# Kernel tuning notes

Measured on AMD Instinct MI355X. Metric: run time of the kernel, lower is better.

## Reference

```python
import jax, jax.numpy as jnp
import numpy as np

N_EMBD = 1024
N_HEAD = 16
HEAD_SIZE = 64

def setup_inputs() -> dict:
    key = jax.random.key(0)
    ks = jax.random.split(key, 6)
    B, T = 4, 2048
    x = jax.random.normal(ks[0], (B, T, N_EMBD), dtype=jnp.float32)
    s = 1.0 / np.sqrt(N_EMBD)
    Wq = jax.random.normal(ks[1], (N_HEAD, N_EMBD, HEAD_SIZE), dtype=jnp.float32) * s
    Wk = jax.random.normal(ks[2], (N_HEAD, N_EMBD, HEAD_SIZE), dtype=jnp.float32) * s
    Wv = jax.random.normal(ks[3], (N_HEAD, N_EMBD, HEAD_SIZE), dtype=jnp.float32) * s
    Wp = jax.random.normal(ks[4], (N_EMBD, N_EMBD), dtype=jnp.float32) * s
    bp = jax.random.normal(ks[5], (N_EMBD,), dtype=jnp.float32) * 0.01
    return {"x": x, "Wq": Wq, "Wk": Wk, "Wv": Wv, "Wp": Wp, "bp": bp}

def reference(x, Wq, Wk, Wv, Wp, bp):
    B, T, C = x.shape
    # per-head projections, all heads at once: [B,H,T,hs]
    q = jnp.einsum('btc,hcd->bhtd', x, Wq)
    k = jnp.einsum('btc,hcd->bhtd', x, Wk)
    v = jnp.einsum('btc,hcd->bhtd', x, Wv)
    # NOTE: original scales by C**-0.5 with C = n_embd (not head_size)
    scale = C ** (-0.5)
    wei = jnp.einsum('bhtd,bhsd->bhts', q, k) * scale  # [B,H,T,T]
    causal = jnp.tril(jnp.ones((T, T), dtype=bool))
    wei = jnp.where(causal, wei, -jnp.inf)
    wei = jax.nn.softmax(wei, axis=-1)
    out = jnp.einsum('bhts,bhsd->bhtd', wei, v)  # [B,H,T,hs]
    out = out.transpose(0, 2, 1, 3).reshape(B, T, -1)  # concat heads -> [B,T,C]
    return out @ Wp + bp
```

## Files before the change

kernel.cpp:

```cpp
#include <hip/hip_runtime.h>
#include <stdint.h>
#include <math.h>

typedef short s16x8 __attribute__((ext_vector_type(8)));
typedef float f32x4 __attribute__((ext_vector_type(4)));
typedef float f32x16 __attribute__((ext_vector_type(16)));

__device__ __forceinline__ unsigned short f2bf(float f) {
    union { float f; uint32_t u; } x; x.f = f;
    uint32_t r = x.u + 0x7FFFu + ((x.u >> 16) & 1u);
    return (unsigned short)(r >> 16);
}

__device__ __forceinline__ uint32_t cvtpk_bf16(float lo, float hi) {
    uint32_t r;
    asm("v_cvt_pk_bf16_f32 %0, %1, %2" : "=v"(r) : "v"(lo), "v"(hi));
    return r;
}

#define GLD_LDS16(gp, lp) __builtin_amdgcn_global_load_lds( \
    (const __attribute__((address_space(1))) uint32_t*)(gp), \
    (__attribute__((address_space(3))) uint32_t*)(lp), 16, 0, 0)

#define MFMA16x16x32(a, b, c) __builtin_amdgcn_mfma_f32_16x16x32_bf16((a), (b), (c), 0, 0, 0)
#define MFMA32x32x16(a, b, c) __builtin_amdgcn_mfma_f32_32x32x16_bf16((a), (b), (c), 0, 0, 0)

__device__ __forceinline__ void plswap(uint32_t a, uint32_t b, int lh, uint32_t& x, uint32_t& y) {
#if __has_builtin(__builtin_amdgcn_permlane32_swap)
    auto r = __builtin_amdgcn_permlane32_swap(a, b, false, false);
    x = (uint32_t)r[0]; y = (uint32_t)r[1];
#else
    uint32_t as = (uint32_t)__shfl_xor((int)a, 32, 64);
    uint32_t bs = (uint32_t)__shfl_xor((int)b, 32, 64);
    x = lh ? bs : a;
    y = lh ? b : as;
#endif
}

__global__ void cvt_x_kernel(const float* __restrict__ x, unsigned short* __restrict__ xb, int n) {
    int i = (blockIdx.x * blockDim.x + threadIdx.x) * 4;
    if (i >= n) return;
    float4 v = *(const float4*)(x + i);
    unsigned short o0 = f2bf(v.x), o1 = f2bf(v.y), o2 = f2bf(v.z), o3 = f2bf(v.w);
    uint64_t packed = (uint64_t)o0 | ((uint64_t)o1 << 16) | ((uint64_t)o2 << 32) | ((uint64_t)o3 << 48);
    *(uint64_t*)(xb + i) = packed;
}

__global__ void cvt_w_kernel(const float* __restrict__ Wq, const float* __restrict__ Wk,
                             const float* __restrict__ Wv, const float* __restrict__ Wp,
                             unsigned short* __restrict__ WtQKV, unsigned short* __restrict__ WtP) {
    int id = (blockIdx.x * blockDim.x + threadIdx.x) * 4;
    int which = id >> 20, rem = id & 1048575;
    const float* src = (which == 0) ? Wq : (which == 1) ? Wk : (which == 2) ? Wv : Wp;
    float4 v = *(const float4*)(src + rem);
    unsigned short* dst;
    if (which < 3) {
        int h = rem >> 16, c = (rem >> 6) & 1023, d = rem & 63;
        dst = WtQKV + (size_t)(which * 1024 + h * 64 + d) * 1024 + c;
    } else {
        int c = rem >> 10, n = rem & 1023;
        dst = WtP + (size_t)n * 1024 + c;
    }
    dst[0] = f2bf(v.x); dst[1024] = f2bf(v.y); dst[2048] = f2bf(v.z); dst[3072] = f2bf(v.w);
}

__global__ __launch_bounds__(512, 4) void gemm_qkv_kernel(
    const unsigned short* __restrict__ A, const unsigned short* __restrict__ Bt,
    unsigned short* __restrict__ qkv2, unsigned short* __restrict__ vT)
{
    constexpr int K = 1024, NT = 32;
    __shared__ __align__(16) unsigned short LA[3][128 * 32];
    __shared__ __align__(16) unsigned short LB[3][256 * 32];

    const int t = threadIdx.x, w = t >> 6, l = t & 63, lr = l & 15, lg = l >> 4;
    const int wm2 = w >> 2, wn4 = w & 3;

    int bid = blockIdx.x;
    int swz = (bid & 7) * 96 + (bid >> 3);
    const int bm = (swz & 63) << 7, bn = (swz >> 6) << 8;

    const unsigned short* Ab = A + (size_t)bm * K;
    const unsigned short* Bb = Bt + (size_t)bn * K;

    int sArow, sAce, sBrow[2], sBce[2];
    {
        int u = t >> 4, x = (t & 15) ^ (u & 15);
        sArow = 4 * u + (x >> 2); sAce = (x & 3) << 3;
        #pragma unroll
        for (int i2 = 0; i2 < 2; ++i2) {
            int i = t + i2 * 512;
            int ub = i >> 4, xb2 = (i & 15) ^ (ub & 15);
            sBrow[i2] = 4 * ub + (xb2 >> 2); sBce[i2] = (xb2 & 3) << 3;
        }
    }

    int aoff[4], boff[4];
    #pragma unroll
    for (int m = 0; m < 4; ++m) {
        int u = 16 * wm2 + 4 * m + (lr >> 2);
        aoff[m] = u * 256 + (((lg + 4 * (lr & 3)) ^ (u & 15)) << 4);
    }
    #pragma unroll
    for (int n = 0; n < 4; ++n) {
        int u = 16 * wn4 + 4 * n + (lr >> 2);
        boff[n] = u * 256 + (((lg + 4 * (lr & 3)) ^ (u & 15)) << 4);
    }

    f32x4 acc[4][4] = {};

    GLD_LDS16(Ab + (size_t)sArow * K + 0 + sAce, &LA[0][t * 8]);
    #pragma unroll
    for (int i2 = 0; i2 < 2; ++i2)
        GLD_LDS16(Bb + (size_t)sBrow[i2] * K + 0 + sBce[i2], &LB[0][(t + i2 * 512) * 8]);
    GLD_LDS16(Ab + (size_t)sArow * K + 32 + sAce, &LA[1][t * 8]);
    #pragma unroll
    for (int i2 = 0; i2 < 2; ++i2)
        GLD_LDS16(Bb + (size_t)sBrow[i2] * K + 32 + sBce[i2], &LB[1][(t + i2 * 512) * 8]);
    asm volatile("s_waitcnt vmcnt(3)" ::: "memory");
    __builtin_amdgcn_sched_barrier(0);
    __builtin_amdgcn_s_barrier();

    int cur = 0;
    for (int j = 0; j < NT; ++j) {
        const int dst = (cur >= 1) ? cur - 1 : cur + 2;
        const bool st = (j + 2 < NT);
        const int k2 = (j + 2) << 5;
        s16x8 af[4], bfr[4];
        #pragma unroll
        for (int m = 0; m < 4; ++m)
            af[m] = *(const s16x8*)((const char*)LA[cur] + aoff[m]);
        #pragma unroll
        for (int n = 0; n < 4; ++n)
            bfr[n] = *(const s16x8*)((const char*)LB[cur] + boff[n]);
        if (st) {
            GLD_LDS16(Ab + (size_t)sArow * K + k2 + sAce, &LA[dst][t * 8]);
            #pragma unroll
            for (int i2 = 0; i2 < 2; ++i2)
                GLD_LDS16(Bb + (size_t)sBrow[i2] * K + k2 + sBce[i2], &LB[dst][(t + i2 * 512) * 8]);
        }
        __builtin_amdgcn_s_barrier();
        asm volatile("s_waitcnt lgkmcnt(0)" ::: "memory");
        __builtin_amdgcn_sched_barrier(0);
        __builtin_amdgcn_s_setprio(1);
        #pragma unroll
        for (int m = 0; m < 4; ++m)
            #pragma unroll
            for (int n = 0; n < 4; ++n)
                acc[m][n] = MFMA16x16x32(af[m], bfr[n], acc[m][n]);
        __builtin_amdgcn_s_setprio(0);
        if (j + 1 < NT) {
            if (st) { asm volatile("s_waitcnt vmcnt(3)" ::: "memory"); }
            else    { asm volatile("s_waitcnt vmcnt(0)" ::: "memory"); }
            __builtin_amdgcn_sched_barrier(0);
        }
        __builtin_amdgcn_s_barrier();
        cur = (cur == 2) ? 0 : cur + 1;
    }

    const bool isV = (bn >= 2048);
    const float sc = (bn < 1024) ? (0.03125f * 1.44269504088896341f) : 1.0f;
    #pragma unroll
    for (int mi = 0; mi < 4; ++mi)
        #pragma unroll
        for (int ni = 0; ni < 4; ++ni) {
            int col = bn + wn4 * 64 + ni * 16 + lr;
            int row0 = bm + wm2 * 64 + mi * 16 + lg * 4;
            if (!isV) {
                #pragma unroll
                for (int r = 0; r < 4; ++r)
                    qkv2[(size_t)(row0 + r) * 2048 + col] = f2bf(acc[mi][ni][r] * sc);
            } else {
                int h = (col >> 6) & 15, d = col & 63;
                size_t vb = ((size_t)((row0 >> 11) * 16 + h) * 64 + d) * 2048 + (row0 & 2047);
                uint32_t u0 = (uint32_t)f2bf(acc[mi][ni][0]) | ((uint32_t)f2bf(acc[mi][ni][1]) << 16);
                uint32_t u1 = (uint32_t)f2bf(acc[mi][ni][2]) | ((uint32_t)f2bf(acc[mi][ni][3]) << 16);
                *(uint32_t*)&vT[vb]     = u0;
                *(uint32_t*)&vT[vb + 2] = u1;
            }
        }
}

__global__ __launch_bounds__(256) void gemm_proj_kernel(
    const unsigned short* __restrict__ A, const unsigned short* __restrict__ Bt,
    float* __restrict__ C, const float* __restrict__ bias, int M, int N, int K)
{
    constexpr int BK = 64;
    __shared__ __align__(16) unsigned short As[128 * BK];
    __shared__ __align__(16) unsigned short Bs[128 * BK];
    const int t = threadIdx.x, w = t >> 6, l = t & 63, lr = l & 15, lg = l >> 4;
    const int wm = (w >> 1) << 6, wn = (w & 1) << 6;
    const int bm = blockIdx.x << 7, bn = blockIdx.y << 7;
    const unsigned short* Ab = A + (size_t)bm * K;
    const unsigned short* Bb = Bt + (size_t)bn * K;
    f32x4 acc[4][4] = {};
    for (int k0 = 0; k0 < K; k0 += BK) {
        __syncthreads();
        #pragma unroll
        for (int i = 0; i < 4; ++i) {
            int c = i * 256 + t;
            GLD_LDS16(Ab + (size_t)(c >> 3) * K + k0 + ((c & 7) << 3), As + c * 8);
        }
        #pragma unroll
        for (int i = 0; i < 4; ++i) {
            int c = i * 256 + t;
            GLD_LDS16(Bb + (size_t)(c >> 3) * K + k0 + ((c & 7) << 3), Bs + c * 8);
        }
        __syncthreads();
        #pragma unroll
        for (int ks = 0; ks < 2; ++ks) {
            s16x8 af[4], bfr[4];
            #pragma unroll
            for (int mi = 0; mi < 4; ++mi)
                af[mi] = *(const s16x8*)&As[(wm + mi * 16 + lr) * BK + ks * 32 + lg * 8];
            #pragma unroll
            for (int ni = 0; ni < 4; ++ni)
                bfr[ni] = *(const s16x8*)&Bs[(wn + ni * 16 + lr) * BK + ks * 32 + lg * 8];
            #pragma unroll
            for (int mi = 0; mi < 4; ++mi)
                #pragma unroll
                for (int ni = 0; ni < 4; ++ni)
                    acc[mi][ni] = MFMA16x16x32(af[mi], bfr[ni], acc[mi][ni]);
        }
    }
    #pragma unroll
    for (int mi = 0; mi < 4; ++mi)
        #pragma unroll
        for (int ni = 0; ni < 4; ++ni) {
            int col = bn + wn + ni * 16 + lr;
            float bv = bias[col];
            #pragma unroll
            for (int r = 0; r < 4; ++r) {
                int row = bm + wm + mi * 16 + lg * 4 + r;
                C[(size_t)row * N + col] = acc[mi][ni][r] + bv;
            }
        }
}

__device__ __forceinline__ void proc32(
    const unsigned short* __restrict__ Ksb, const unsigned short* __restrict__ Vtb,
    const s16x8* qf, f32x16* o, float& m_r, f32x16& l_acc, s16x8 onesf,
    int qms, bool domask, int lq, int lh)
{
    const int ub = lq >> 1;
    const int vb8 = (lq & 1) << 3;
    f32x16 S[2] = {};
    __builtin_amdgcn_s_setprio(1);
    #pragma unroll
    for (int sblk = 0; sblk < 2; ++sblk)
        #pragma unroll
        for (int kd = 0; kd < 4; ++kd) {
            s16x8 kf = *(const s16x8*)((const char*)Ksb + (sblk * 16 + ub) * 256
                                       + ((((2 * kd + lh) + vb8) ^ ub) << 4));
            S[sblk] = MFMA32x32x16(kf, qf[kd], S[sblk]);
        }
    __builtin_amdgcn_s_setprio(0);
    if (domask) {
        #pragma unroll
        for (int sblk = 0; sblk < 2; ++sblk)
            #pragma unroll
            for (int r = 0; r < 16; ++r) {
                int s_loc = sblk * 32 + (r & 3) + 8 * (r >> 2) + 4 * lh;
                S[sblk][r] = (s_loc <= qms) ? S[sblk][r] : -1e30f;
            }
    }
    float zm = S[0][0];
    #pragma unroll
    for (int r = 1; r < 15; r += 2) zm = fmaxf(fmaxf(zm, S[0][r]), S[0][r + 1]);
    zm = fmaxf(zm, S[0][15]);
    #pragma unroll
    for (int r = 0; r < 16; r += 2) zm = fmaxf(fmaxf(zm, S[1][r]), S[1][r + 1]);
    zm = fmaxf(zm, __shfl_xor(zm, 32, 64));
    const bool defer = (__all(zm <= m_r + 8.0f) != 0);
    if (!defer) {
        float mn = fmaxf(m_r, zm);
        float alpha = exp2f(m_r - mn);
        m_r = mn;
        l_acc[0] *= alpha;
        o[0] *= alpha;
        o[1] *= alpha;
    }
    uint32_t pk[2][8];
    #pragma unroll
    for (int sblk = 0; sblk < 2; ++sblk) {
        #pragma unroll
        for (int r = 0; r < 16; ++r)
            S[sblk][r] = exp2f(S[sblk][r] - m_r);
        #pragma unroll
        for (int hh = 0; hh < 8; ++hh)
            pk[sblk][hh] = cvtpk_bf16(S[sblk][2 * hh], S[sblk][2 * hh + 1]);
    }
    s16x8 pf[4];
    #pragma unroll
    for (int ks2 = 0; ks2 < 4; ++ks2) {
        int sb = ks2 >> 1, Bh = 4 * (ks2 & 1);
        uint32_t w0, w1, w2, w3;
        plswap(pk[sb][Bh + 0], pk[sb][Bh + 2], lh, w0, w2);
        plswap(pk[sb][Bh + 1], pk[sb][Bh + 3], lh, w1, w3);
        union { uint32_t u[4]; s16x8 v; } pu;
        pu.u[0] = w0; pu.u[1] = w1; pu.u[2] = w2; pu.u[3] = w3;
        pf[ks2] = pu.v;
    }
    __builtin_amdgcn_s_setprio(1);
    #pragma unroll
    for (int dblk = 0; dblk < 2; ++dblk)
        #pragma unroll
        for (int ks2 = 0; ks2 < 4; ++ks2) {
            s16x8 vf = *(const s16x8*)((const char*)Vtb + (dblk * 16 + ub) * 256
                                       + ((((2 * ks2 + lh) + vb8) ^ ub) << 4));
            o[dblk] = MFMA32x32x16(vf, pf[ks2], o[dblk]);
        }
    #pragma unroll
    for (int ks2 = 0; ks2 < 4; ++ks2)
        l_acc = MFMA32x32x16(onesf, pf[ks2], l_acc);
    __builtin_amdgcn_s_setprio(0);
}

__global__ __launch_bounds__(256, 4) void attn_kernel(
    const unsigned short* __restrict__ qkv2, const unsigned short* __restrict__ vT,
    unsigned short* __restrict__ attnO, int T)
{
    __shared__ __align__(16) unsigned short Ks[2][64 * 64];
    __shared__ __align__(16) unsigned short Vt[2][64 * 64];

    const int i = blockIdx.x;
    const int g = i & 7, j = i >> 3;
    const int tq = 15 - (j >> 3);
    const int bh = ((j & 7) << 3) | g;
    const int b = bh >> 4, h = bh & 15;
    const int nkv = 2 * tq + 2;

    const int t = threadIdx.x, w = t >> 6, l = t & 63, lq = l & 31, lh = l >> 5;
    const int c0 = tq * 128 + 32 * w;
    const int lastT = (c0 + 31) >> 6;

    const unsigned short* qbase = qkv2 + (size_t)b * T * 2048;
    const unsigned short* kbase = qbase + 1024 + h * 64;
    const unsigned short* vtb   = vT + (size_t)(b * 16 + h) * 64 * 2048;

    s16x8 qf[4];
    #pragma unroll
    for (int kd = 0; kd < 4; ++kd)
        qf[kd] = *(const s16x8*)(qbase + (size_t)(c0 + lq) * 2048 + h * 64 + kd * 16 + lh * 8);

    f32x16 o[2] = {}, l_acc = {};
    float m_r = -1e30f;
    s16x8 onesf;
    {
        union { uint32_t u[4]; s16x8 v; } ou;
        #pragma unroll
        for (int k2 = 0; k2 < 4; ++k2) ou.u[k2] = 0x3F803F80u;
        onesf = ou.v;
    }

    int srow[2], sch[2];
    #pragma unroll
    for (int i2 = 0; i2 < 2; ++i2) {
        int c = t + i2 * 256;
        int su = c >> 4, sx = (c & 15) ^ (su & 15);
        srow[i2] = 2 * su + (sx >> 3); sch[i2] = (sx & 7) << 3;
    }
    auto STAGE = [&](int buf, int s0) {
        #pragma unroll
        for (int i2 = 0; i2 < 2; ++i2) {
            int c = t + i2 * 256;
            GLD_LDS16(kbase + (size_t)(s0 + srow[i2]) * 2048 + sch[i2], &Ks[buf][c * 8]);
            GLD_LDS16(vtb + (size_t)srow[i2] * 2048 + s0 + sch[i2], &Vt[buf][c * 8]);
        }
    };

    STAGE(0, 0);
    __syncthreads();

    for (int kt = 0; kt < nkv; ++kt) {
        const int cur = kt & 1, nxt = cur ^ 1;
        if (kt + 1 < nkv) STAGE(nxt, (kt + 1) * 64);
        if (kt <= lastT)
            proc32(Ks[cur], Vt[cur], qf, o, m_r, l_acc, onesf,
                   c0 + lq - kt * 64, kt == lastT, lq, lh);
        __syncthreads();
    }

    {
        float inv = 1.0f / l_acc[0];
        #pragma unroll
        for (int dblk = 0; dblk < 2; ++dblk)
            #pragma unroll
            for (int r = 0; r < 16; r += 2) {
                int d = dblk * 32 + (r & 3) + 8 * (r >> 2) + 4 * lh;
                uint32_t ua = cvtpk_bf16(o[dblk][r] * inv, o[dblk][r + 1] * inv);
                *(uint32_t*)&attnO[(size_t)(b * T + c0 + lq) * 1024 + h * 64 + d] = ua;
            }
    }
}

extern "C" void kernel_launch(void* const* d_in, const int* in_sizes, int n_in,
                              void* d_out, int out_size, void* d_ws, size_t ws_size,
                              hipStream_t stream) {
    const float* x  = (const float*)d_in[0];
    const float* Wq = (const float*)d_in[1];
    const float* Wk = (const float*)d_in[2];
    const float* Wv = (const float*)d_in[3];
    const float* Wp = (const float*)d_in[4];
    const float* bp = (const float*)d_in[5];
    float* out = (float*)d_out;

    const int T = 2048, C = 1024;
    const int BT = in_sizes[0] / C;
    const int B  = BT / T;

    char* ws = (char*)d_ws;
    unsigned short* xb    = (unsigned short*)(ws);
    unsigned short* WtQKV = (unsigned short*)(ws + 16777216);
    unsigned short* WtP   = (unsigned short*)(ws + 23068672);
    unsigned short* qkv2  = (unsigned short*)(ws + 25165824);
    unsigned short* vT    = (unsigned short*)(ws + 58720256);
    unsigned short* attn  = (unsigned short*)(ws + 75497472);
    (void)ws_size; (void)n_in; (void)out_size;

    cvt_x_kernel<<<(BT * C / 4 + 255) / 256, 256, 0, stream>>>(x, xb, BT * C);
    cvt_w_kernel<<<4096, 256, 0, stream>>>(Wq, Wk, Wv, Wp, WtQKV, WtP);

    gemm_qkv_kernel<<<768, 512, 0, stream>>>(xb, WtQKV, qkv2, vT);

    attn_kernel<<<B * 16 * 16, 256, 0, stream>>>(qkv2, vT, attn, T);

    gemm_proj_kernel<<<dim3(BT / 128, 1024 / 128), 256, 0, stream>>>(
        attn, WtP, out, bp, BT, 1024, C);
}
```

Before: 203.2 us.

## Reuse pipelined QKV GEMM for output projection and fuse conversion kernels

The simple output-projection GEMM (128x128 tiles, 256 threads, no pipelining) is replaced by a templated version of the triple-buffered, swizzled QKV GEMM with 128x256 tiles and a bias epilogue. The x and weight bf16 conversion kernels are merged into a single launch. The aim is better MFMA utilisation in the projection and one less kernel launch, at the cost of fewer blocks (256) for the projection GEMM, which may underfill the GPU.

```diff
diff --git a/kernel.cpp b/kernel.cpp
--- a/kernel.cpp
+++ b/kernel.cpp
@@ -37,19 +37,22 @@
 #endif
 }
 
-__global__ void cvt_x_kernel(const float* __restrict__ x, unsigned short* __restrict__ xb, int n) {
-    int i = (blockIdx.x * blockDim.x + threadIdx.x) * 4;
-    if (i >= n) return;
-    float4 v = *(const float4*)(x + i);
-    unsigned short o0 = f2bf(v.x), o1 = f2bf(v.y), o2 = f2bf(v.z), o3 = f2bf(v.w);
-    uint64_t packed = (uint64_t)o0 | ((uint64_t)o1 << 16) | ((uint64_t)o2 << 32) | ((uint64_t)o3 << 48);
-    *(uint64_t*)(xb + i) = packed;
-}
-
-__global__ void cvt_w_kernel(const float* __restrict__ Wq, const float* __restrict__ Wk,
-                             const float* __restrict__ Wv, const float* __restrict__ Wp,
-                             unsigned short* __restrict__ WtQKV, unsigned short* __restrict__ WtP) {
-    int id = (blockIdx.x * blockDim.x + threadIdx.x) * 4;
+__global__ void cvt_all_kernel(const float* __restrict__ x,
+                               const float* __restrict__ Wq, const float* __restrict__ Wk,
+                               const float* __restrict__ Wv, const float* __restrict__ Wp,
+                               unsigned short* __restrict__ xb,
+                               unsigned short* __restrict__ WtQKV, unsigned short* __restrict__ WtP,
+                               int xunits) {
+    int u = blockIdx.x * blockDim.x + threadIdx.x;
+    if (u < xunits) {
+        int i = u * 4;
+        float4 v = *(const float4*)(x + i);
+        unsigned short o0 = f2bf(v.x), o1 = f2bf(v.y), o2 = f2bf(v.z), o3 = f2bf(v.w);
+        uint64_t packed = (uint64_t)o0 | ((uint64_t)o1 << 16) | ((uint64_t)o2 << 32) | ((uint64_t)o3 << 48);
+        *(uint64_t*)(xb + i) = packed;
+        return;
+    }
+    int id = (u - xunits) * 4;
     int which = id >> 20, rem = id & 1048575;
     const float* src = (which == 0) ? Wq : (which == 1) ? Wk : (which == 2) ? Wv : Wp;
     float4 v = *(const float4*)(src + rem);
@@ -64,9 +67,11 @@
     dst[0] = f2bf(v.x); dst[1024] = f2bf(v.y); dst[2048] = f2bf(v.z); dst[3072] = f2bf(v.w);
 }
 
-__global__ __launch_bounds__(512, 4) void gemm_qkv_kernel(
+template<int MODE, int CPX>
+__global__ __launch_bounds__(512, 4) void gemm_dp_kernel(
     const unsigned short* __restrict__ A, const unsigned short* __restrict__ Bt,
-    unsigned short* __restrict__ qkv2, unsigned short* __restrict__ vT)
+    void* __restrict__ Cout, unsigned short* __restrict__ vT,
+    const float* __restrict__ bias)
 {
     constexpr int K = 1024, NT = 32;
     __shared__ __align__(16) unsigned short LA[3][128 * 32];
@@ -76,7 +81,7 @@
     const int wm2 = w >> 2, wn4 = w & 3;
 
     int bid = blockIdx.x;
-    int swz = (bid & 7) * 96 + (bid >> 3);
+    int swz = (bid & 7) * CPX + (bid >> 3);
     const int bm = (swz & 63) << 7, bn = (swz >> 6) << 8;
 
     const unsigned short* Ab = A + (size_t)bm * K;
@@ -157,83 +162,43 @@
         cur = (cur == 2) ? 0 : cur + 1;
     }
 
-    const bool isV = (bn >= 2048);
-    const float sc = (bn < 1024) ? (0.03125f * 1.44269504088896341f) : 1.0f;
-    #pragma unroll
-    for (int mi = 0; mi < 4; ++mi)
-        #pragma unroll
-        for (int ni = 0; ni < 4; ++ni) {
-            int col = bn + wn4 * 64 + ni * 16 + lr;
-            int row0 = bm + wm2 * 64 + mi * 16 + lg * 4;
-            if (!isV) {
+    if (MODE == 1) {
+        float* C = (float*)Cout;
+        #pragma unroll
+        for (int mi = 0; mi < 4; ++mi)
+            #pragma unroll
+            for (int ni = 0; ni < 4; ++ni) {
+                int col = bn + wn4 * 64 + ni * 16 + lr;
+                float bv = bias[col];
+                int row0 = bm + wm2 * 64 + mi * 16 + lg * 4;
                 #pragma unroll
                 for (int r = 0; r < 4; ++r)
-                    qkv2[(size_t)(row0 + r) * 2048 + col] = f2bf(acc[mi][ni][r] * sc);
-            } else {
-                int h = (col >> 6) & 15, d = col & 63;
-                size_t vb = ((size_t)((row0 >> 11) * 16 + h) * 64 + d) * 2048 + (row0 & 2047);
-                uint32_t u0 = (uint32_t)f2bf(acc[mi][ni][0]) | ((uint32_t)f2bf(acc[mi][ni][1]) << 16);
-                uint32_t u1 = (uint32_t)f2bf(acc[mi][ni][2]) | ((uint32_t)f2bf(acc[mi][ni][3]) << 16);
-                *(uint32_t*)&vT[vb]     = u0;
-                *(uint32_t*)&vT[vb + 2] = u1;
+                    C[(size_t)(row0 + r) * 1024 + col] = acc[mi][ni][r] + bv;
             }
-        }
-}
-
-__global__ __launch_bounds__(256) void gemm_proj_kernel(
-    const unsigned short* __restrict__ A, const unsigned short* __restrict__ Bt,
-    float* __restrict__ C, const float* __restrict__ bias, int M, int N, int K)
-{
-    constexpr int BK = 64;
-    __shared__ __align__(16) unsigned short As[128 * BK];
-    __shared__ __align__(16) unsigned short Bs[128 * BK];
-    const int t = threadIdx.x, w = t >> 6, l = t & 63, lr = l & 15, lg = l >> 4;
-    const int wm = (w >> 1) << 6, wn = (w & 1) << 6;
-    const int bm = blockIdx.x << 7, bn = blockIdx.y << 7;
-    const unsigned short* Ab = A + (size_t)bm * K;
-    const unsigned short* Bb = Bt + (size_t)bn * K;
-    f32x4 acc[4][4] = {};
-    for (int k0 = 0; k0 < K; k0 += BK) {
-        __syncthreads();
-        #pragma unroll
-        for (int i = 0; i < 4; ++i) {
-            int c = i * 256 + t;
-            GLD_LDS16(Ab + (size_t)(c >> 3) * K + k0 + ((c & 7) << 3), As + c * 8);
-        }
-        #pragma unroll
-        for (int i = 0; i < 4; ++i) {
-            int c = i * 256 + t;
-            GLD_LDS16(Bb + (size_t)(c >> 3) * K + k0 + ((c & 7) << 3), Bs + c * 8);
-        }
-        __syncthreads();
-        #pragma unroll
-        for (int ks = 0; ks < 2; ++ks) {
-            s16x8 af[4], bfr[4];
-            #pragma unroll
-            for (int mi = 0; mi < 4; ++mi)
-                af[mi] = *(const s16x8*)&As[(wm + mi * 16 + lr) * BK + ks * 32 + lg * 8];
-            #pragma unroll
-            for (int ni = 0; ni < 4; ++ni)
-                bfr[ni] = *(const s16x8*)&Bs[(wn + ni * 16 + lr) * BK + ks * 32 + lg * 8];
-            #pragma unroll
-            for (int mi = 0; mi < 4; ++mi)
-                #pragma unroll
-                for (int ni = 0; ni < 4; ++ni)
-                    acc[mi][ni] = MFMA16x16x32(af[mi], bfr[ni], acc[mi][ni]);
-        }
-    }
-    #pragma unroll
-    for (int mi = 0; mi < 4; ++mi)
-        #pragma unroll
-        for (int ni = 0; ni < 4; ++ni) {
-            int col = bn + wn + ni * 16 + lr;
-            float bv = bias[col];
-            #pragma unroll
-            for (int r = 0; r < 4; ++r) {
-                int row = bm + wm + mi * 16 + lg * 4 + r;
-                C[(size_t)row * N + col] = acc[mi][ni][r] + bv;
+    } else {
+        unsigned short* qkv2 = (unsigned short*)Cout;
+        const bool isV = (bn >= 2048);
+        const float sc = (bn < 1024) ? (0.03125f * 1.44269504088896341f) : 1.0f;
+        #pragma unroll
+        for (int mi = 0; mi < 4; ++mi)
+            #pragma unroll
+            for (int ni = 0; ni < 4; ++ni) {
+                int col = bn + wn4 * 64 + ni * 16 + lr;
+                int row0 = bm + wm2 * 64 + mi * 16 + lg * 4;
+                if (!isV) {
+                    #pragma unroll
+                    for (int r = 0; r < 4; ++r)
+                        qkv2[(size_t)(row0 + r) * 2048 + col] = f2bf(acc[mi][ni][r] * sc);
+                } else {
+                    int h = (col >> 6) & 15, d = col & 63;
+                    size_t vb = ((size_t)((row0 >> 11) * 16 + h) * 64 + d) * 2048 + (row0 & 2047);
+                    uint32_t u0 = (uint32_t)f2bf(acc[mi][ni][0]) | ((uint32_t)f2bf(acc[mi][ni][1]) << 16);
+                    uint32_t u1 = (uint32_t)f2bf(acc[mi][ni][2]) | ((uint32_t)f2bf(acc[mi][ni][3]) << 16);
+                    *(uint32_t*)&vT[vb]     = u0;
+                    *(uint32_t*)&vT[vb + 2] = u1;
+                }
             }
-        }
+    }
 }
 
 __device__ __forceinline__ void proc32(
@@ -417,13 +382,14 @@
     unsigned short* attn  = (unsigned short*)(ws + 75497472);
     (void)ws_size; (void)n_in; (void)out_size;
 
-    cvt_x_kernel<<<(BT * C / 4 + 255) / 256, 256, 0, stream>>>(x, xb, BT * C);
-    cvt_w_kernel<<<4096, 256, 0, stream>>>(Wq, Wk, Wv, Wp, WtQKV, WtP);
-
-    gemm_qkv_kernel<<<768, 512, 0, stream>>>(xb, WtQKV, qkv2, vT);
+    const int xunits = BT * C / 4;
+    const int wunits = 4 * 1024 * 1024 / 4;
+    cvt_all_kernel<<<(xunits + wunits) / 256, 256, 0, stream>>>(
+        x, Wq, Wk, Wv, Wp, xb, WtQKV, WtP, xunits);
+
+    gemm_dp_kernel<0, 96><<<768, 512, 0, stream>>>(xb, WtQKV, qkv2, vT, nullptr);
 
     attn_kernel<<<B * 16 * 16, 256, 0, stream>>>(qkv2, vT, attn, T);
 
-    gemm_proj_kernel<<<dim3(BT / 128, 1024 / 128), 256, 0, stream>>>(
-        attn, WtP, out, bp, BT, 1024, C);
-}
+    gemm_dp_kernel<1, 32><<<256, 512, 0, stream>>>(attn, WtP, out, nullptr, bp);
+}
```

Result: faster. 198.4 us (-2.4%).
